# Kernel optimization log

Hardware: AMD Instinct MI355X
Metric: run time of the kernel (lower is better)

Reference implementation:

```python
import jax, jax.numpy as jnp
import numpy as np


def setup_inputs() -> dict:
    key = jax.random.key(0)
    ks = jax.random.split(key, 8)
    B, L, E, D, A = 128, 196, 2048, 1024, 1024
    s_e = 1.0 / np.sqrt(E)
    s_d = 1.0 / np.sqrt(D)
    return {
        "encoder_outputs": jax.random.normal(ks[0], (B, L, E), jnp.float32),
        "decoder_hidden": jax.random.normal(ks[1], (B, D), jnp.float32),
        "Wq": jax.random.normal(ks[2], (A, E), jnp.float32) * s_e,
        "bq": jax.random.normal(ks[3], (A,), jnp.float32) * s_e,
        "Wv": jax.random.normal(ks[4], (A, E), jnp.float32) * s_e,
        "bv": jax.random.normal(ks[5], (A,), jnp.float32) * s_e,
        "Wd": jax.random.normal(ks[6], (A, D), jnp.float32) * s_d,
        "bd": jax.random.normal(ks[7], (A,), jnp.float32) * s_d,
    }


def reference(encoder_outputs, decoder_hidden, Wq, bq, Wv, bv, Wd, bd):
    # get_encoder_features: project encoder outputs to queries/values [B, L, A]
    enc_q = jnp.einsum('ble,ae->bla', encoder_outputs, Wq) + bq
    enc_v = jnp.einsum('ble,ae->bla', encoder_outputs, Wv) + bv
    # forward: project decoder hidden [B, A]
    dec_q = decoder_hidden @ Wd.T + bd
    # attn_energy = bmm(enc_q, dec_q) -> [B, L]; tanh then softmax over L
    energy = jnp.tanh(jnp.einsum('bla,ba->bl', enc_q, dec_q))
    weights = jax.nn.softmax(energy, axis=1)
    # context = bmm(weights, enc_v) -> [B, A]
    context = jnp.einsum('bl,bla->ba', weights, enc_v)
    return context
```

## Files before the change

### kernel.cpp

```cpp
#include <hip/hip_runtime.h>
#include <cstdint>
#include <cstddef>


template <bool BNC>
__global__ __launch_bounds__(256) void gemm_part(
    const float* __restrict__ A, const float* __restrict__ Bm,
    float* __restrict__ part, int M, int N, int K, int kPerZ) {
  __shared__ float As[32][132];
  __shared__ float Bs[32][132];
  const int t = threadIdx.x;
  const int tx = t & 15, ty = t >> 4;
  const int n0 = blockIdx.x * 128;
  const int m0 = blockIdx.y * 128;
  const int z  = blockIdx.z;
  const int k0 = z * kPerZ;

  float acc[8][8];
#pragma unroll
  for (int i = 0; i < 8; ++i)
#pragma unroll
    for (int j = 0; j < 8; ++j) acc[i][j] = 0.f;

  for (int kb = k0; kb < k0 + kPerZ; kb += 32) {
    __syncthreads();
    {
      int m = t >> 1, kq = (t & 1) * 16;
      const float* src = A + (size_t)(m0 + m) * K + (kb + kq);
      float4 v0 = *(const float4*)(src + 0);
      float4 v1 = *(const float4*)(src + 4);
      float4 v2 = *(const float4*)(src + 8);
      float4 v3 = *(const float4*)(src + 12);
      As[kq + 0][m] = v0.x; As[kq + 1][m] = v0.y; As[kq + 2][m] = v0.z; As[kq + 3][m] = v0.w;
      As[kq + 4][m] = v1.x; As[kq + 5][m] = v1.y; As[kq + 6][m] = v1.z; As[kq + 7][m] = v1.w;
      As[kq + 8][m] = v2.x; As[kq + 9][m] = v2.y; As[kq + 10][m] = v2.z; As[kq + 11][m] = v2.w;
      As[kq + 12][m] = v3.x; As[kq + 13][m] = v3.y; As[kq + 14][m] = v3.z; As[kq + 15][m] = v3.w;
    }
    if (BNC) {
      int kk = t >> 3, nq = (t & 7) * 16;
      const float* src = Bm + (size_t)(kb + kk) * N + (n0 + nq);
      float4 v0 = *(const float4*)(src + 0);
      float4 v1 = *(const float4*)(src + 4);
      float4 v2 = *(const float4*)(src + 8);
      float4 v3 = *(const float4*)(src + 12);
      *(float4*)&Bs[kk][nq + 0] = v0;
      *(float4*)&Bs[kk][nq + 4] = v1;
      *(float4*)&Bs[kk][nq + 8] = v2;
      *(float4*)&Bs[kk][nq + 12] = v3;
    } else {
      int n = t >> 1, kq = (t & 1) * 16;
      const float* src = Bm + (size_t)(n0 + n) * K + (kb + kq);
      float4 v0 = *(const float4*)(src + 0);
      float4 v1 = *(const float4*)(src + 4);
      float4 v2 = *(const float4*)(src + 8);
      float4 v3 = *(const float4*)(src + 12);
      Bs[kq + 0][n] = v0.x; Bs[kq + 1][n] = v0.y; Bs[kq + 2][n] = v0.z; Bs[kq + 3][n] = v0.w;
      Bs[kq + 4][n] = v1.x; Bs[kq + 5][n] = v1.y; Bs[kq + 6][n] = v1.z; Bs[kq + 7][n] = v1.w;
      Bs[kq + 8][n] = v2.x; Bs[kq + 9][n] = v2.y; Bs[kq + 10][n] = v2.z; Bs[kq + 11][n] = v2.w;
      Bs[kq + 12][n] = v3.x; Bs[kq + 13][n] = v3.y; Bs[kq + 14][n] = v3.z; Bs[kq + 15][n] = v3.w;
    }
    __syncthreads();
#pragma unroll 4
    for (int kk = 0; kk < 32; ++kk) {
      float av[8], bv[8];
      *(float4*)&av[0] = *(const float4*)&As[kk][ty * 8 + 0];
      *(float4*)&av[4] = *(const float4*)&As[kk][ty * 8 + 4];
      *(float4*)&bv[0] = *(const float4*)&Bs[kk][tx * 8 + 0];
      *(float4*)&bv[4] = *(const float4*)&Bs[kk][tx * 8 + 4];
#pragma unroll
      for (int i = 0; i < 8; ++i)
#pragma unroll
        for (int j = 0; j < 8; ++j) acc[i][j] = fmaf(av[i], bv[j], acc[i][j]);
    }
  }
  float* dst = part + (size_t)z * M * N;
#pragma unroll
  for (int i = 0; i < 8; ++i) {
    int m = m0 + ty * 8 + i;
    float4 lo = make_float4(acc[i][0], acc[i][1], acc[i][2], acc[i][3]);
    float4 hi = make_float4(acc[i][4], acc[i][5], acc[i][6], acc[i][7]);
    *(float4*)&dst[(size_t)m * N + n0 + tx * 8 + 0] = lo;
    *(float4*)&dst[(size_t)m * N + n0 + tx * 8 + 4] = hi;
  }
}

__global__ __launch_bounds__(256) void reduce_part(
    const float* __restrict__ part, const float* __restrict__ bias,
    float* __restrict__ out, int MN, int N, int Z) {
  int i = blockIdx.x * 256 + threadIdx.x;
  if (i * 4 >= MN) return;
  float4 a = make_float4(0.f, 0.f, 0.f, 0.f);
  for (int z = 0; z < Z; ++z) {
    float4 v = *(const float4*)&part[(size_t)z * MN + i * 4];
    a.x += v.x; a.y += v.y; a.z += v.z; a.w += v.w;
  }
  if (bias) {
    int n = (i * 4) % N;
    float4 bb = *(const float4*)&bias[n];
    a.x += bb.x; a.y += bb.y; a.z += bb.z; a.w += bb.w;
  }
  *(float4*)&out[(size_t)i * 4] = a;
}

__global__ __launch_bounds__(512) void attn_pass(
    const float* __restrict__ x,
    const float* __restrict__ u,
    const float* __restrict__ dec_q,
    const float* __restrict__ bq,
    float* __restrict__ Yp,
    float* __restrict__ ms) {
  const int L = 196, E = 2048, A = 1024, RPB = 49;
  __shared__ float uS[2048];
  __shared__ float eS[8];
  __shared__ float red[8];
  const int t = threadIdx.x;
  const int lane = t & 63, w = t >> 6;
  const int b = blockIdx.x >> 2, q = blockIdx.x & 3;
  const int l0 = q * RPB, lend = l0 + RPB;

  *(float4*)&uS[t * 4] = *(const float4*)&u[(size_t)b * E + t * 4];

  {
    const float* dq = dec_q + (size_t)b * A;
    float cp = fmaf(bq[t], dq[t], bq[t + 512] * dq[t + 512]);
    for (int off = 32; off; off >>= 1) cp += __shfl_xor(cp, off);
    if (lane == 0) red[w] = cp;
  }
  __syncthreads();
  const float cB = red[0] + red[1] + red[2] + red[3] + red[4] + red[5] + red[6] + red[7];

  float m = -1e30f, s = 0.f;
  float4 y = make_float4(0.f, 0.f, 0.f, 0.f);

  for (int lb = l0; lb < lend; lb += 8) {
    int l = lb + w;
    float e = -1e30f;
    if (l < lend) {
      const float* xr = x + ((size_t)b * L + l) * E;
      float d = 0.f;
#pragma unroll
      for (int i = 0; i < 8; ++i) {
        float4 xv = *(const float4*)(xr + lane * 4 + i * 256);
        float4 uv = *(const float4*)&uS[lane * 4 + i * 256];
        d = fmaf(xv.x, uv.x, d);
        d = fmaf(xv.y, uv.y, d);
        d = fmaf(xv.z, uv.z, d);
        d = fmaf(xv.w, uv.w, d);
      }
      for (int off = 32; off; off >>= 1) d += __shfl_xor(d, off);
      e = tanhf(d + cB);
    }
    if (lane == 0) eS[w] = e;
    __syncthreads();

    float ev[8];
#pragma unroll
    for (int j = 0; j < 8; ++j) ev[j] = eS[j];
    float bm = ev[0];
#pragma unroll
    for (int j = 1; j < 8; ++j) bm = fmaxf(bm, ev[j]);
    float mn = fmaxf(m, bm);
    float r = __expf(m - mn);
    s *= r;
    y.x *= r; y.y *= r; y.z *= r; y.w *= r;
#pragma unroll
    for (int j = 0; j < 8; ++j) {
      int l2 = lb + j;
      if (l2 < lend) {
        float wj = __expf(ev[j] - mn);
        s += wj;
        float4 xv = *(const float4*)(x + ((size_t)b * L + l2) * E + t * 4);
        y.x = fmaf(wj, xv.x, y.x);
        y.y = fmaf(wj, xv.y, y.y);
        y.z = fmaf(wj, xv.z, y.z);
        y.w = fmaf(wj, xv.w, y.w);
      }
    }
    m = mn;
    __syncthreads();
  }

  *(float4*)&Yp[(size_t)(b * 4 + q) * E + t * 4] = y;
  if (t == 0) {
    ms[(b * 4 + q) * 2 + 0] = m;
    ms[(b * 4 + q) * 2 + 1] = s;
  }
}

__global__ __launch_bounds__(256) void merge_y(
    const float* __restrict__ Yp, const float* __restrict__ ms,
    float* __restrict__ y) {
  const int E = 2048;
  int b = blockIdx.x, t = threadIdx.x;
  float mq[4], sq[4];
#pragma unroll
  for (int q = 0; q < 4; ++q) {
    mq[q] = ms[(b * 4 + q) * 2 + 0];
    sq[q] = ms[(b * 4 + q) * 2 + 1];
  }
  float M = fmaxf(fmaxf(mq[0], mq[1]), fmaxf(mq[2], mq[3]));
  float al[4], S = 0.f;
#pragma unroll
  for (int q = 0; q < 4; ++q) {
    al[q] = __expf(mq[q] - M);
    S = fmaf(sq[q], al[q], S);
  }
  float inv = 1.f / S;
#pragma unroll
  for (int half = 0; half < 2; ++half) {
    int pos = t * 4 + half * 1024;
    float4 a = make_float4(0.f, 0.f, 0.f, 0.f);
#pragma unroll
    for (int q = 0; q < 4; ++q) {
      float4 v = *(const float4*)&Yp[(size_t)(b * 4 + q) * E + pos];
      a.x = fmaf(al[q], v.x, a.x);
      a.y = fmaf(al[q], v.y, a.y);
      a.z = fmaf(al[q], v.z, a.z);
      a.w = fmaf(al[q], v.w, a.w);
    }
    a.x *= inv; a.y *= inv; a.z *= inv; a.w *= inv;
    *(float4*)&y[(size_t)b * E + pos] = a;
  }
}

extern "C" void kernel_launch(void* const* d_in, const int* in_sizes, int n_in,
                              void* d_out, int out_size, void* d_ws, size_t ws_size,
                              hipStream_t stream) {
  const float* x  = (const float*)d_in[0];
  const float* dh = (const float*)d_in[1];
  const float* Wq = (const float*)d_in[2];
  const float* bq = (const float*)d_in[3];
  const float* Wv = (const float*)d_in[4];
  const float* bv = (const float*)d_in[5];
  const float* Wd = (const float*)d_in[6];
  const float* bd = (const float*)d_in[7];
  float* out = (float*)d_out;
  float* ws = (float*)d_ws;

  float* dec_q = ws;
  float* u     = ws + 131072;
  float* y     = ws + 393216;
  float* Yp    = ws + 655360;
  float* msb   = ws + 1703936;
  float* part  = ws + 1705984;

  gemm_part<false><<<dim3(8, 1, 32), 256, 0, stream>>>(dh, Wd, part, 128, 1024, 1024, 32);
  reduce_part<<<dim3(128), 256, 0, stream>>>(part, bd, dec_q, 131072, 1024, 32);
  gemm_part<true><<<dim3(16, 1, 16), 256, 0, stream>>>(dec_q, Wq, part, 128, 2048, 1024, 64);
  reduce_part<<<dim3(256), 256, 0, stream>>>(part, nullptr, u, 262144, 2048, 16);
  attn_pass<<<dim3(512), 512, 0, stream>>>(x, u, dec_q, bq, Yp, msb);
  merge_y<<<dim3(128), 256, 0, stream>>>(Yp, msb, y);
  gemm_part<false><<<dim3(8, 1, 32), 256, 0, stream>>>(y, Wv, part, 128, 1024, 2048, 64);
  reduce_part<<<dim3(128), 256, 0, stream>>>(part, bv, out, 131072, 1024, 32);
}
```

Baseline: 382.3 us.

## Single-read attention pass with register-held rows, drop online-softmax max, narrower GEMM tiles

The attention kernel now loads each encoder row into registers once per wave and reuses it for both the energy dot product and the weighted accumulation. Previously each row was read twice, once per wave for the dot and once by the whole block for the context sum. Because tanh bounds the energy to [-1,1], the running max and rescaling are dropped, so exp(tanh) is accumulated directly and the merge kernel only sums the partials and divides. Waves are reduced through shared memory at the end, and the block size falls to 256 threads, which costs more registers per thread. Separately, the split-K GEMM tile shrinks from 128x128 to 128x64 to launch twice as many blocks.

```diff
diff --git a/kernel.cpp b/kernel.cpp
--- a/kernel.cpp
+++ b/kernel.cpp
@@ -8,17 +8,17 @@
     const float* __restrict__ A, const float* __restrict__ Bm,
     float* __restrict__ part, int M, int N, int K, int kPerZ) {
   __shared__ float As[32][132];
-  __shared__ float Bs[32][132];
+  __shared__ float Bs[32][68];
   const int t = threadIdx.x;
-  const int tx = t & 15, ty = t >> 4;
-  const int n0 = blockIdx.x * 128;
+  const int tx = t & 7, ty = t >> 3;
+  const int n0 = blockIdx.x * 64;
   const int m0 = blockIdx.y * 128;
   const int z  = blockIdx.z;
   const int k0 = z * kPerZ;
 
-  float acc[8][8];
-#pragma unroll
-  for (int i = 0; i < 8; ++i)
+  float acc[4][8];
+#pragma unroll
+  for (int i = 0; i < 4; ++i)
 #pragma unroll
     for (int j = 0; j < 8; ++j) acc[i][j] = 0.f;
 
@@ -37,46 +37,37 @@
       As[kq + 12][m] = v3.x; As[kq + 13][m] = v3.y; As[kq + 14][m] = v3.z; As[kq + 15][m] = v3.w;
     }
     if (BNC) {
-      int kk = t >> 3, nq = (t & 7) * 16;
+      int kk = t >> 3, nq = (t & 7) * 8;
       const float* src = Bm + (size_t)(kb + kk) * N + (n0 + nq);
       float4 v0 = *(const float4*)(src + 0);
       float4 v1 = *(const float4*)(src + 4);
-      float4 v2 = *(const float4*)(src + 8);
-      float4 v3 = *(const float4*)(src + 12);
       *(float4*)&Bs[kk][nq + 0] = v0;
       *(float4*)&Bs[kk][nq + 4] = v1;
-      *(float4*)&Bs[kk][nq + 8] = v2;
-      *(float4*)&Bs[kk][nq + 12] = v3;
     } else {
-      int n = t >> 1, kq = (t & 1) * 16;
+      int n = t >> 2, kq = (t & 3) * 8;
       const float* src = Bm + (size_t)(n0 + n) * K + (kb + kq);
       float4 v0 = *(const float4*)(src + 0);
       float4 v1 = *(const float4*)(src + 4);
-      float4 v2 = *(const float4*)(src + 8);
-      float4 v3 = *(const float4*)(src + 12);
       Bs[kq + 0][n] = v0.x; Bs[kq + 1][n] = v0.y; Bs[kq + 2][n] = v0.z; Bs[kq + 3][n] = v0.w;
       Bs[kq + 4][n] = v1.x; Bs[kq + 5][n] = v1.y; Bs[kq + 6][n] = v1.z; Bs[kq + 7][n] = v1.w;
-      Bs[kq + 8][n] = v2.x; Bs[kq + 9][n] = v2.y; Bs[kq + 10][n] = v2.z; Bs[kq + 11][n] = v2.w;
-      Bs[kq + 12][n] = v3.x; Bs[kq + 13][n] = v3.y; Bs[kq + 14][n] = v3.z; Bs[kq + 15][n] = v3.w;
     }
     __syncthreads();
 #pragma unroll 4
     for (int kk = 0; kk < 32; ++kk) {
-      float av[8], bv[8];
-      *(float4*)&av[0] = *(const float4*)&As[kk][ty * 8 + 0];
-      *(float4*)&av[4] = *(const float4*)&As[kk][ty * 8 + 4];
+      float av[4], bv[8];
+      *(float4*)&av[0] = *(const float4*)&As[kk][ty * 4];
       *(float4*)&bv[0] = *(const float4*)&Bs[kk][tx * 8 + 0];
       *(float4*)&bv[4] = *(const float4*)&Bs[kk][tx * 8 + 4];
 #pragma unroll
-      for (int i = 0; i < 8; ++i)
+      for (int i = 0; i < 4; ++i)
 #pragma unroll
         for (int j = 0; j < 8; ++j) acc[i][j] = fmaf(av[i], bv[j], acc[i][j]);
     }
   }
   float* dst = part + (size_t)z * M * N;
 #pragma unroll
-  for (int i = 0; i < 8; ++i) {
-    int m = m0 + ty * 8 + i;
+  for (int i = 0; i < 4; ++i) {
+    int m = m0 + ty * 4 + i;
     float4 lo = make_float4(acc[i][0], acc[i][1], acc[i][2], acc[i][3]);
     float4 hi = make_float4(acc[i][4], acc[i][5], acc[i][6], acc[i][7]);
     *(float4*)&dst[(size_t)m * N + n0 + tx * 8 + 0] = lo;
@@ -102,121 +93,102 @@
   *(float4*)&out[(size_t)i * 4] = a;
 }
 
-__global__ __launch_bounds__(512) void attn_pass(
+__global__ __launch_bounds__(256) void attn_pass(
     const float* __restrict__ x,
     const float* __restrict__ u,
     const float* __restrict__ dec_q,
     const float* __restrict__ bq,
     float* __restrict__ Yp,
-    float* __restrict__ ms) {
+    float* __restrict__ ss) {
   const int L = 196, E = 2048, A = 1024, RPB = 49;
-  __shared__ float uS[2048];
-  __shared__ float eS[8];
-  __shared__ float red[8];
+  __shared__ float yS[4][2048];
+  __shared__ float red[4];
+  __shared__ float sred[4];
   const int t = threadIdx.x;
   const int lane = t & 63, w = t >> 6;
   const int b = blockIdx.x >> 2, q = blockIdx.x & 3;
-  const int l0 = q * RPB, lend = l0 + RPB;
-
-  *(float4*)&uS[t * 4] = *(const float4*)&u[(size_t)b * E + t * 4];
+  const int l0 = q * RPB;
 
   {
     const float* dq = dec_q + (size_t)b * A;
-    float cp = fmaf(bq[t], dq[t], bq[t + 512] * dq[t + 512]);
+    float cp = 0.f;
+#pragma unroll
+    for (int j = 0; j < 4; ++j) cp = fmaf(bq[t + j * 256], dq[t + j * 256], cp);
     for (int off = 32; off; off >>= 1) cp += __shfl_xor(cp, off);
     if (lane == 0) red[w] = cp;
   }
   __syncthreads();
-  const float cB = red[0] + red[1] + red[2] + red[3] + red[4] + red[5] + red[6] + red[7];
-
-  float m = -1e30f, s = 0.f;
-  float4 y = make_float4(0.f, 0.f, 0.f, 0.f);
-
-  for (int lb = l0; lb < lend; lb += 8) {
-    int l = lb + w;
-    float e = -1e30f;
-    if (l < lend) {
-      const float* xr = x + ((size_t)b * L + l) * E;
-      float d = 0.f;
-#pragma unroll
-      for (int i = 0; i < 8; ++i) {
-        float4 xv = *(const float4*)(xr + lane * 4 + i * 256);
-        float4 uv = *(const float4*)&uS[lane * 4 + i * 256];
-        d = fmaf(xv.x, uv.x, d);
-        d = fmaf(xv.y, uv.y, d);
-        d = fmaf(xv.z, uv.z, d);
-        d = fmaf(xv.w, uv.w, d);
-      }
-      for (int off = 32; off; off >>= 1) d += __shfl_xor(d, off);
-      e = tanhf(d + cB);
-    }
-    if (lane == 0) eS[w] = e;
-    __syncthreads();
-
-    float ev[8];
-#pragma unroll
-    for (int j = 0; j < 8; ++j) ev[j] = eS[j];
-    float bm = ev[0];
-#pragma unroll
-    for (int j = 1; j < 8; ++j) bm = fmaxf(bm, ev[j]);
-    float mn = fmaxf(m, bm);
-    float r = __expf(m - mn);
-    s *= r;
-    y.x *= r; y.y *= r; y.z *= r; y.w *= r;
-#pragma unroll
-    for (int j = 0; j < 8; ++j) {
-      int l2 = lb + j;
-      if (l2 < lend) {
-        float wj = __expf(ev[j] - mn);
-        s += wj;
-        float4 xv = *(const float4*)(x + ((size_t)b * L + l2) * E + t * 4);
-        y.x = fmaf(wj, xv.x, y.x);
-        y.y = fmaf(wj, xv.y, y.y);
-        y.z = fmaf(wj, xv.z, y.z);
-        y.w = fmaf(wj, xv.w, y.w);
-      }
-    }
-    m = mn;
-    __syncthreads();
-  }
-
-  *(float4*)&Yp[(size_t)(b * 4 + q) * E + t * 4] = y;
-  if (t == 0) {
-    ms[(b * 4 + q) * 2 + 0] = m;
-    ms[(b * 4 + q) * 2 + 1] = s;
-  }
+  const float cB = red[0] + red[1] + red[2] + red[3];
+
+  float4 ur[8];
+  const float* ub = u + (size_t)b * E;
+#pragma unroll
+  for (int i = 0; i < 8; ++i) ur[i] = *(const float4*)(ub + lane * 4 + i * 256);
+
+  float4 y[8];
+#pragma unroll
+  for (int i = 0; i < 8; ++i) y[i] = make_float4(0.f, 0.f, 0.f, 0.f);
+  float s = 0.f;
+
+  for (int l = l0 + w; l < l0 + RPB; l += 4) {
+    const float* xr = x + ((size_t)b * L + l) * E;
+    float4 xv[8];
+#pragma unroll
+    for (int i = 0; i < 8; ++i) xv[i] = *(const float4*)(xr + lane * 4 + i * 256);
+    float d = 0.f;
+#pragma unroll
+    for (int i = 0; i < 8; ++i) {
+      d = fmaf(xv[i].x, ur[i].x, d);
+      d = fmaf(xv[i].y, ur[i].y, d);
+      d = fmaf(xv[i].z, ur[i].z, d);
+      d = fmaf(xv[i].w, ur[i].w, d);
+    }
+    for (int off = 32; off; off >>= 1) d += __shfl_xor(d, off);
+    float wj = __expf(tanhf(d + cB));
+    s += wj;
+#pragma unroll
+    for (int i = 0; i < 8; ++i) {
+      y[i].x = fmaf(wj, xv[i].x, y[i].x);
+      y[i].y = fmaf(wj, xv[i].y, y[i].y);
+      y[i].z = fmaf(wj, xv[i].z, y[i].z);
+      y[i].w = fmaf(wj, xv[i].w, y[i].w);
+    }
+  }
+
+#pragma unroll
+  for (int i = 0; i < 8; ++i) *(float4*)&yS[w][lane * 4 + i * 256] = y[i];
+  if (lane == 0) sred[w] = s;
+  __syncthreads();
+
+#pragma unroll
+  for (int h = 0; h < 2; ++h) {
+    int pos = t * 4 + h * 1024;
+    float4 a0 = *(const float4*)&yS[0][pos];
+    float4 a1 = *(const float4*)&yS[1][pos];
+    float4 a2 = *(const float4*)&yS[2][pos];
+    float4 a3 = *(const float4*)&yS[3][pos];
+    float4 a = make_float4(a0.x + a1.x + a2.x + a3.x, a0.y + a1.y + a2.y + a3.y,
+                           a0.z + a1.z + a2.z + a3.z, a0.w + a1.w + a2.w + a3.w);
+    *(float4*)&Yp[(size_t)blockIdx.x * E + pos] = a;
+  }
+  if (t == 0) ss[blockIdx.x] = sred[0] + sred[1] + sred[2] + sred[3];
 }
 
 __global__ __launch_bounds__(256) void merge_y(
-    const float* __restrict__ Yp, const float* __restrict__ ms,
+    const float* __restrict__ Yp, const float* __restrict__ ss,
     float* __restrict__ y) {
   const int E = 2048;
   int b = blockIdx.x, t = threadIdx.x;
-  float mq[4], sq[4];
-#pragma unroll
-  for (int q = 0; q < 4; ++q) {
-    mq[q] = ms[(b * 4 + q) * 2 + 0];
-    sq[q] = ms[(b * 4 + q) * 2 + 1];
-  }
-  float M = fmaxf(fmaxf(mq[0], mq[1]), fmaxf(mq[2], mq[3]));
-  float al[4], S = 0.f;
-#pragma unroll
-  for (int q = 0; q < 4; ++q) {
-    al[q] = __expf(mq[q] - M);
-    S = fmaf(sq[q], al[q], S);
-  }
+  float S = ss[b * 4 + 0] + ss[b * 4 + 1] + ss[b * 4 + 2] + ss[b * 4 + 3];
   float inv = 1.f / S;
 #pragma unroll
-  for (int half = 0; half < 2; ++half) {
-    int pos = t * 4 + half * 1024;
+  for (int h = 0; h < 2; ++h) {
+    int pos = t * 4 + h * 1024;
     float4 a = make_float4(0.f, 0.f, 0.f, 0.f);
 #pragma unroll
-    for (int q = 0; q < 4; ++q) {
-      float4 v = *(const float4*)&Yp[(size_t)(b * 4 + q) * E + pos];
-      a.x = fmaf(al[q], v.x, a.x);
-      a.y = fmaf(al[q], v.y, a.y);
-      a.z = fmaf(al[q], v.z, a.z);
-      a.w = fmaf(al[q], v.w, a.w);
+    for (int qq = 0; qq < 4; ++qq) {
+      float4 v = *(const float4*)&Yp[(size_t)(b * 4 + qq) * E + pos];
+      a.x += v.x; a.y += v.y; a.z += v.z; a.w += v.w;
     }
     a.x *= inv; a.y *= inv; a.z *= inv; a.w *= inv;
     *(float4*)&y[(size_t)b * E + pos] = a;
@@ -241,15 +213,15 @@
   float* u     = ws + 131072;
   float* y     = ws + 393216;
   float* Yp    = ws + 655360;
-  float* msb   = ws + 1703936;
+  float* ssb   = ws + 1703936;
   float* part  = ws + 1705984;
 
-  gemm_part<false><<<dim3(8, 1, 32), 256, 0, stream>>>(dh, Wd, part, 128, 1024, 1024, 32);
+  gemm_part<false><<<dim3(16, 1, 32), 256, 0, stream>>>(dh, Wd, part, 128, 1024, 1024, 32);
   reduce_part<<<dim3(128), 256, 0, stream>>>(part, bd, dec_q, 131072, 1024, 32);
-  gemm_part<true><<<dim3(16, 1, 16), 256, 0, stream>>>(dec_q, Wq, part, 128, 2048, 1024, 64);
+  gemm_part<true><<<dim3(32, 1, 16), 256, 0, stream>>>(dec_q, Wq, part, 128, 2048, 1024, 64);
   reduce_part<<<dim3(256), 256, 0, stream>>>(part, nullptr, u, 262144, 2048, 16);
-  attn_pass<<<dim3(512), 512, 0, stream>>>(x, u, dec_q, bq, Yp, msb);
-  merge_y<<<dim3(128), 256, 0, stream>>>(Yp, msb, y);
-  gemm_part<false><<<dim3(8, 1, 32), 256, 0, stream>>>(y, Wv, part, 128, 1024, 2048, 64);
+  attn_pass<<<dim3(512), 256, 0, stream>>>(x, u, dec_q, bq, Yp, ssb);
+  merge_y<<<dim3(128), 256, 0, stream>>>(Yp, ssb, y);
+  gemm_part<false><<<dim3(16, 1, 32), 256, 0, stream>>>(y, Wv, part, 128, 1024, 2048, 64);
   reduce_part<<<dim3(128), 256, 0, stream>>>(part, bv, out, 131072, 1024, 32);
 }
```

After: 368.8 us. 3.5% less time.
